# Performance work log

Hardware: AMD Instinct MI355X
Metric: run time of the kernel (lower is better)

## Reference

```python
import jax, jax.numpy as jnp
import numpy as np

B, T, C = 4, 4096, 512
H, KS = 8, 9
D = C // H
PAD = KS // 2


def setup_inputs() -> dict:
    key = jax.random.key(0)
    ks = jax.random.split(key, 9)
    s = 1.0 / np.sqrt(C)
    return {
        "x": jax.random.normal(ks[0], (B, T, C), jnp.float32),
        "Wq": jax.random.normal(ks[1], (C, C), jnp.float32) * s,
        "bq": jax.random.normal(ks[2], (C,), jnp.float32) * 0.01,
        "Wk": jax.random.normal(ks[3], (C, C), jnp.float32) * s,
        "bk": jax.random.normal(ks[4], (C,), jnp.float32) * 0.01,
        "Wv": jax.random.normal(ks[5], (C, C), jnp.float32) * s,
        "bv": jax.random.normal(ks[6], (C,), jnp.float32) * 0.01,
        "Wo": jax.random.normal(ks[7], (C, C), jnp.float32) * s,
        "bo": jax.random.normal(ks[8], (C,), jnp.float32) * 0.01,
    }


def reference(x, Wq, bq, Wk, bk, Wv, bv, Wo, bo):
    Bx, Tx, Cx = x.shape
    # projections (torch Linear: x @ W.T + b), split heads -> (B,H,T,D)
    q = (x @ Wq.T + bq).reshape(Bx, Tx, H, D).transpose(0, 2, 1, 3)
    k = (x @ Wk.T + bk).reshape(Bx, Tx, H, D).transpose(0, 2, 1, 3)
    v = (x @ Wv.T + bv).reshape(Bx, Tx, H, D).transpose(0, 2, 1, 3)
    # replicate-pad along time (matches F.pad mode='replicate')
    k_pad = jnp.pad(k, ((0, 0), (0, 0), (PAD, PAD), (0, 0)), mode='edge')
    v_pad = jnp.pad(v, ((0, 0), (0, 0), (PAD, PAD), (0, 0)), mode='edge')
    # window gather indices: (T, KS) into padded time axis
    idx = jnp.arange(Tx)[:, None] + jnp.arange(KS)[None, :]
    k_unf = k_pad[:, :, idx, :]  # (B,H,T,KS,D)
    v_unf = v_pad[:, :, idx, :]  # (B,H,T,KS,D)
    scale = 1.0 / np.sqrt(D)
    scores = jnp.einsum('bhtd,bhtkd->bhtk', q, k_unf) * scale  # (B,H,T,KS)
    attn = jax.nn.softmax(scores, axis=-1)
    y = jnp.einsum('bhtk,bhtkd->bhtd', attn, v_unf)  # (B,H,T,D)
    y = y.transpose(0, 2, 1, 3).reshape(Bx, Tx, Cx)
    return y @ Wo.T + bo
```

## Files before the change

kernel.cpp:

```cpp
#include <hip/hip_runtime.h>
#include <hip/hip_bf16.h>

#define B_    4
#define T_    4096
#define C_    512
#define H_    8
#define D_    64
#define KS_   9
#define PAD_  4
#define MTOT  (B_ * T_)
#define PLANE (MTOT * C_)
#define WU    (C_ * C_ / 8)

typedef __bf16 bf16_t;
typedef __bf16 bf16x8 __attribute__((ext_vector_type(8)));
typedef float  f32x4  __attribute__((ext_vector_type(4)));
typedef unsigned int  uint2v __attribute__((ext_vector_type(2)));

__global__ __launch_bounds__(256)
void conv_all(const float* __restrict__ Wq, const float* __restrict__ Wk,
              const float* __restrict__ Wv, const float* __restrict__ Wo,
              const float* __restrict__ x,
              bf16_t* __restrict__ Wb, bf16_t* __restrict__ xb) {
  int i = blockIdx.x * 256 + threadIdx.x;
  const float* src;
  bf16_t* dst;
  if (i < 4 * WU) {
    int w = i >> 15;
    const float* W = (w == 0) ? Wq : (w == 1) ? Wk : (w == 2) ? Wv : Wo;
    src = W + (size_t)(i & (WU - 1)) * 8;
    dst = Wb + (size_t)i * 8;
  } else {
    size_t j = (size_t)(i - 4 * WU);
    src = x + j * 8;
    dst = xb + j * 8;
  }
  float4 f0 = ((const float4*)src)[0];
  float4 f1 = ((const float4*)src)[1];
  bf16x8 o;
  o[0] = (bf16_t)f0.x; o[1] = (bf16_t)f0.y; o[2] = (bf16_t)f0.z; o[3] = (bf16_t)f0.w;
  o[4] = (bf16_t)f1.x; o[5] = (bf16_t)f1.y; o[6] = (bf16_t)f1.z; o[7] = (bf16_t)f1.w;
  *(bf16x8*)dst = o;
}

#define BM   128
#define BN   128
#define BK   32
#define NKT  (C_ / BK)
#define ASL  (BM * BK)
#define SLOT (2 * ASL)

#define GLD(srcp, off) __builtin_amdgcn_global_load_lds(                     \
    (const __attribute__((address_space(1))) unsigned int*)(srcp),           \
    (__attribute__((address_space(3))) unsigned int*)(&sm[off]), 16, 0, 0)

template<int MODE>
__global__ __launch_bounds__(256, 4)
void gemm8p(const bf16_t* __restrict__ A, const bf16_t* __restrict__ Bw,
            const float* __restrict__ b0, const float* __restrict__ b1,
            const float* __restrict__ b2, void* __restrict__ Outp) {
  __shared__ __align__(16) bf16_t sm[2 * SLOT];

  constexpr int GX  = (MODE == 0) ? (3 * C_ / BN) : (C_ / BN);
  constexpr int NWG = GX * (MTOT / BM);
  constexpr int CPX = NWG / 8;

  const int ord = blockIdx.y * GX + blockIdx.x;
  const int lg  = (ord & 7) * CPX + (ord >> 3);
  const int n0  = (lg % GX) * BN;
  const int m0  = (lg / GX) * BM;

  const int tid  = threadIdx.x;
  const int lane = tid & 63;
  const int wave = tid >> 6;
  const int wm   = wave >> 1;
  const int wn   = wave & 1;
  const int lr   = lane & 15;
  const int lq   = lane >> 4;

  const bf16_t* aSrc[2];
  const bf16_t* bSrc[2];
#pragma unroll
  for (int s = 0; s < 2; ++s) {
    int u = s * 256 + tid, r = u >> 2, sl = u & 3;
    int cs = (sl ^ ((r >> 1) & 3)) << 3;
    if constexpr (MODE == 0) {
      aSrc[s] = A + (size_t)(m0 + r) * C_ + cs;
    } else {
      int bb = m0 >> 12, t0 = m0 & (T_ - 1);
      aSrc[s] = A + ((size_t)bb * H_ * T_ + t0 + r) * D_ + cs;
    }
    bSrc[s] = Bw + (size_t)(n0 + r) * C_ + cs;
  }
  auto ofsA = [](int kt) -> size_t {
    if constexpr (MODE == 0) return (size_t)kt * BK;
    else return (size_t)(kt >> 1) * ((size_t)T_ * D_) + (size_t)(kt & 1) * 32;
  };

#pragma unroll
  for (int s = 0; s < 2; ++s) GLD(aSrc[s] + ofsA(0), (s * 256 + tid) * 8);
#pragma unroll
  for (int s = 0; s < 2; ++s) GLD(bSrc[s], ASL + (s * 256 + tid) * 8);
  asm volatile("s_waitcnt vmcnt(0)" ::: "memory");
  __builtin_amdgcn_s_barrier();

  f32x4 acc[4][4] = {};
  const int co = ((lq ^ ((lr >> 1) & 3)) << 3);

#pragma unroll
  for (int kt = 0; kt < NKT; ++kt) {
    const int rsl = kt & 1;
    const int wof = ((kt + 1) & 1) * SLOT;
    const bf16_t* abase = &sm[rsl * SLOT + (wm * 64 + lr) * BK + co];
    const bf16_t* bbase = &sm[rsl * SLOT + ASL + (wn * 64 + lr) * BK + co];

    bf16x8 af[4], bfr[4];
#pragma unroll
    for (int i = 0; i < 4; ++i) {
      af[i]  = *(const bf16x8*)(abase + i * (16 * BK));
      bfr[i] = *(const bf16x8*)(bbase + i * (16 * BK));
    }
    if (kt + 1 < NKT) {
#pragma unroll
      for (int s = 0; s < 2; ++s)
        GLD(aSrc[s] + ofsA(kt + 1), wof + (s * 256 + tid) * 8);
#pragma unroll
      for (int s = 0; s < 2; ++s)
        GLD(bSrc[s] + (size_t)(kt + 1) * BK, wof + ASL + (s * 256 + tid) * 8);
    }
    __builtin_amdgcn_s_setprio(1);
#pragma unroll
    for (int i = 0; i < 4; ++i)
#pragma unroll
      for (int j = 0; j < 4; ++j)
        acc[i][j] = __builtin_amdgcn_mfma_f32_16x16x32_bf16(
            bfr[j], af[i], acc[i][j], 0, 0, 0);
    __builtin_amdgcn_s_setprio(0);
    if (kt + 1 < NKT) {
      asm volatile("s_waitcnt vmcnt(0)" ::: "memory");
      __builtin_amdgcn_s_barrier();
    }
  }

  const int tl = lane & 15;
  const int dq = (lane >> 4) << 2;
  if constexpr (MODE == 0) {
    const int z  = n0 >> 9;
    const float* bias = (z == 0) ? b0 : (z == 1) ? b1 : b2;
    const int bb = m0 >> 12;
    const int t0 = m0 & (T_ - 1);
    bf16_t* plane = (bf16_t*)Outp + (size_t)z * PLANE;
#pragma unroll
    for (int j = 0; j < 4; ++j) {
      const int cc = (n0 & (C_ - 1)) + wn * 64 + j * 16 + dq;
      const int hh = cc >> 6, dd = cc & 63;
      const float4 bq4 = *(const float4*)(bias + cc);
      bf16_t* hb = plane + ((size_t)(bb * H_ + hh) * T_) * D_ + dd;
#pragma unroll
      for (int i = 0; i < 4; ++i) {
        const int t = t0 + wm * 64 + i * 16 + tl;
        bf16_t v0 = (bf16_t)(acc[i][j][0] + bq4.x);
        bf16_t v1 = (bf16_t)(acc[i][j][1] + bq4.y);
        bf16_t v2 = (bf16_t)(acc[i][j][2] + bq4.z);
        bf16_t v3 = (bf16_t)(acc[i][j][3] + bq4.w);
        unsigned int lo = ((unsigned short*)&v0)[0] |
                          ((unsigned int)((unsigned short*)&v1)[0] << 16);
        unsigned int hi = ((unsigned short*)&v2)[0] |
                          ((unsigned int)((unsigned short*)&v3)[0] << 16);
        uint2v pk; pk[0] = lo; pk[1] = hi;
        *(uint2v*)(hb + (size_t)t * D_) = pk;
      }
    }
  } else {
    float* outp = (float*)Outp;
#pragma unroll
    for (int j = 0; j < 4; ++j) {
      const int n = n0 + wn * 64 + j * 16 + dq;
      const float4 bq4 = *(const float4*)(b0 + n);
#pragma unroll
      for (int i = 0; i < 4; ++i) {
        const int m = m0 + wm * 64 + i * 16 + tl;
        float4 v;
        v.x = acc[i][j][0] + bq4.x;
        v.y = acc[i][j][1] + bq4.y;
        v.z = acc[i][j][2] + bq4.z;
        v.w = acc[i][j][3] + bq4.w;
        *(float4*)(outp + (size_t)m * C_ + n) = v;
      }
    }
  }
}

__global__ __launch_bounds__(256)
void attn_kernel(const bf16_t* __restrict__ qkv, bf16_t* __restrict__ y) {
  const int tid  = threadIdx.x;
  const int sub  = tid & 7;
  const int tl   = tid >> 3;
  const int t    = blockIdx.x * 32 + tl;
  const int h    = blockIdx.y;
  const int b    = blockIdx.z;

  const size_t pl = (size_t)(b * H_ + h) * T_ * D_;
  const bf16_t* q = qkv + pl;
  const bf16_t* k = qkv + (size_t)PLANE + pl;
  const bf16_t* v = qkv + (size_t)2 * PLANE + pl;
  const int c = sub * 8;

  int tj[KS_];
#pragma unroll
  for (int j = 0; j < KS_; ++j) {
    int tt = t - PAD_ + j;
    tj[j] = tt < 0 ? 0 : (tt >= T_ ? T_ - 1 : tt);
  }

  bf16x8 q8 = *(const bf16x8*)(q + (size_t)t * D_ + c);
  float qf[8];
#pragma unroll
  for (int e = 0; e < 8; ++e) qf[e] = (float)q8[e];

  float s[KS_];
#pragma unroll
  for (int j = 0; j < KS_; ++j) {
    bf16x8 k8 = *(const bf16x8*)(k + (size_t)tj[j] * D_ + c);
    float d0 = 0.f;
#pragma unroll
    for (int e = 0; e < 8; ++e) d0 += qf[e] * (float)k8[e];
    s[j] = d0;
  }

#pragma unroll
  for (int m = 1; m < 8; m <<= 1)
#pragma unroll
    for (int j = 0; j < KS_; ++j) s[j] += __shfl_xor(s[j], m, 8);

  float mx = s[0];
#pragma unroll
  for (int j = 1; j < KS_; ++j) mx = fmaxf(mx, s[j]);
  float w[KS_], sum = 0.f;
#pragma unroll
  for (int j = 0; j < KS_; ++j) {
    w[j] = __expf((s[j] - mx) * 0.125f);
    sum += w[j];
  }
  const float inv = 1.f / sum;
#pragma unroll
  for (int j = 0; j < KS_; ++j) w[j] *= inv;

  float o[8] = {0.f, 0.f, 0.f, 0.f, 0.f, 0.f, 0.f, 0.f};
#pragma unroll
  for (int j = 0; j < KS_; ++j) {
    bf16x8 v8 = *(const bf16x8*)(v + (size_t)tj[j] * D_ + c);
#pragma unroll
    for (int e = 0; e < 8; ++e) o[e] += w[j] * (float)v8[e];
  }
  bf16x8 o8;
#pragma unroll
  for (int e = 0; e < 8; ++e) o8[e] = (bf16_t)o[e];
  *(bf16x8*)(y + pl + (size_t)t * D_ + c) = o8;
}

extern "C" void kernel_launch(void* const* d_in, const int* in_sizes, int n_in,
                              void* d_out, int out_size, void* d_ws, size_t ws_size,
                              hipStream_t stream) {
  const float* x  = (const float*)d_in[0];
  const float* Wq = (const float*)d_in[1];
  const float* bq = (const float*)d_in[2];
  const float* Wk = (const float*)d_in[3];
  const float* bk = (const float*)d_in[4];
  const float* Wv = (const float*)d_in[5];
  const float* bv = (const float*)d_in[6];
  const float* Wo = (const float*)d_in[7];
  const float* bo = (const float*)d_in[8];
  float* out = (float*)d_out;

  bf16_t* Wb  = (bf16_t*)d_ws;
  bf16_t* xb  = Wb + (size_t)4 * C_ * C_;
  bf16_t* qkv = xb + (size_t)PLANE;
  bf16_t* y   = xb;

  conv_all<<<(4 * WU + PLANE / 8) / 256, 256, 0, stream>>>(Wq, Wk, Wv, Wo, x, Wb, xb);
  gemm8p<0><<<dim3(3 * C_ / BN, MTOT / BM), 256, 0, stream>>>(
      xb, Wb, bq, bk, bv, qkv);
  attn_kernel<<<dim3(T_ / 32, H_, B_), 256, 0, stream>>>(qkv, y);
  gemm8p<1><<<dim3(C_ / BN, MTOT / BM), 256, 0, stream>>>(
      y, Wb + (size_t)3 * C_ * C_, bo, nullptr, nullptr, out);
}
```

Measured before the change: 172.2 us.

## Give each wave private LDS tiles to drop block barriers in GEMM

Each wave now loads its own 64-row A and 64-row B slices into a private double-buffered LDS region, with two stages in flight, instead of sharing block-wide tiles. This removes the per-k-step s_barrier and the full vmcnt(0) drain, replacing them with a partial vmcnt wait. The cost is redundant global loads, since waves in the same row or column fetch the same data twice, and four times the LDS per block, so launch bounds drop occupancy from 4 to 2 blocks per CU.

```diff
diff --git a/kernel.cpp b/kernel.cpp
--- a/kernel.cpp
+++ b/kernel.cpp
@@ -47,19 +47,18 @@
 #define BN   128
 #define BK   32
 #define NKT  (C_ / BK)
-#define ASL  (BM * BK)
-#define SLOT (2 * ASL)
+#define WSL  4096
 
 #define GLD(srcp, off) __builtin_amdgcn_global_load_lds(                     \
     (const __attribute__((address_space(1))) unsigned int*)(srcp),           \
     (__attribute__((address_space(3))) unsigned int*)(&sm[off]), 16, 0, 0)
 
 template<int MODE>
-__global__ __launch_bounds__(256, 4)
+__global__ __launch_bounds__(256, 2)
 void gemm8p(const bf16_t* __restrict__ A, const bf16_t* __restrict__ Bw,
             const float* __restrict__ b0, const float* __restrict__ b1,
             const float* __restrict__ b2, void* __restrict__ Outp) {
-  __shared__ __align__(16) bf16_t sm[2 * SLOT];
+  __shared__ __align__(16) bf16_t sm[4 * 2 * WSL];
 
   constexpr int GX  = (MODE == 0) ? (3 * C_ / BN) : (C_ / BN);
   constexpr int NWG = GX * (MTOT / BM);
@@ -77,56 +76,57 @@
   const int wn   = wave & 1;
   const int lr   = lane & 15;
   const int lq   = lane >> 4;
-
-  const bf16_t* aSrc[2];
-  const bf16_t* bSrc[2];
-#pragma unroll
-  for (int s = 0; s < 2; ++s) {
-    int u = s * 256 + tid, r = u >> 2, sl = u & 3;
-    int cs = (sl ^ ((r >> 1) & 3)) << 3;
+  const int wbase = wave * (2 * WSL);
+
+  const bf16_t* aSrc[4];
+  const bf16_t* bSrc[4];
+#pragma unroll
+  for (int s = 0; s < 4; ++s) {
+    int u = s * 64 + lane;
+    int r = u >> 2, ch = u & 3;
+    int cs = (ch ^ ((r >> 1) & 3)) << 3;
     if constexpr (MODE == 0) {
-      aSrc[s] = A + (size_t)(m0 + r) * C_ + cs;
+      aSrc[s] = A + (size_t)(m0 + wm * 64 + r) * C_ + cs;
     } else {
       int bb = m0 >> 12, t0 = m0 & (T_ - 1);
-      aSrc[s] = A + ((size_t)bb * H_ * T_ + t0 + r) * D_ + cs;
-    }
-    bSrc[s] = Bw + (size_t)(n0 + r) * C_ + cs;
+      aSrc[s] = A + ((size_t)bb * H_ * T_ + t0 + wm * 64 + r) * D_ + cs;
+    }
+    bSrc[s] = Bw + (size_t)(n0 + wn * 64 + r) * C_ + cs;
   }
   auto ofsA = [](int kt) -> size_t {
     if constexpr (MODE == 0) return (size_t)kt * BK;
     else return (size_t)(kt >> 1) * ((size_t)T_ * D_) + (size_t)(kt & 1) * 32;
   };
 
-#pragma unroll
-  for (int s = 0; s < 2; ++s) GLD(aSrc[s] + ofsA(0), (s * 256 + tid) * 8);
-#pragma unroll
-  for (int s = 0; s < 2; ++s) GLD(bSrc[s], ASL + (s * 256 + tid) * 8);
-  asm volatile("s_waitcnt vmcnt(0)" ::: "memory");
-  __builtin_amdgcn_s_barrier();
+#define STAGE(kt, sl) do {                                                   \
+    _Pragma("unroll")                                                        \
+    for (int s_ = 0; s_ < 4; ++s_)                                           \
+      GLD(aSrc[s_] + ofsA(kt), wbase + (sl) * WSL + (s_ * 64 + lane) * 8);   \
+    _Pragma("unroll")                                                        \
+    for (int s_ = 0; s_ < 4; ++s_)                                           \
+      GLD(bSrc[s_] + (size_t)(kt) * BK,                                      \
+          wbase + (sl) * WSL + 2048 + (s_ * 64 + lane) * 8);                 \
+  } while (0)
+
+  STAGE(0, 0);
+  STAGE(1, 1);
 
   f32x4 acc[4][4] = {};
   const int co = ((lq ^ ((lr >> 1) & 3)) << 3);
 
 #pragma unroll
   for (int kt = 0; kt < NKT; ++kt) {
-    const int rsl = kt & 1;
-    const int wof = ((kt + 1) & 1) * SLOT;
-    const bf16_t* abase = &sm[rsl * SLOT + (wm * 64 + lr) * BK + co];
-    const bf16_t* bbase = &sm[rsl * SLOT + ASL + (wn * 64 + lr) * BK + co];
-
+    if (kt < NKT - 1) asm volatile("s_waitcnt vmcnt(8)" ::: "memory");
+    else              asm volatile("s_waitcnt vmcnt(0)" ::: "memory");
+    __builtin_amdgcn_sched_barrier(0);
+
+    const bf16_t* ab = &sm[wbase + (kt & 1) * WSL + lr * BK + co];
+    const bf16_t* bb2 = &sm[wbase + (kt & 1) * WSL + 2048 + lr * BK + co];
     bf16x8 af[4], bfr[4];
 #pragma unroll
     for (int i = 0; i < 4; ++i) {
-      af[i]  = *(const bf16x8*)(abase + i * (16 * BK));
-      bfr[i] = *(const bf16x8*)(bbase + i * (16 * BK));
-    }
-    if (kt + 1 < NKT) {
-#pragma unroll
-      for (int s = 0; s < 2; ++s)
-        GLD(aSrc[s] + ofsA(kt + 1), wof + (s * 256 + tid) * 8);
-#pragma unroll
-      for (int s = 0; s < 2; ++s)
-        GLD(bSrc[s] + (size_t)(kt + 1) * BK, wof + ASL + (s * 256 + tid) * 8);
+      af[i]  = *(const bf16x8*)(ab + i * (16 * BK));
+      bfr[i] = *(const bf16x8*)(bb2 + i * (16 * BK));
     }
     __builtin_amdgcn_s_setprio(1);
 #pragma unroll
@@ -136,11 +136,10 @@
         acc[i][j] = __builtin_amdgcn_mfma_f32_16x16x32_bf16(
             bfr[j], af[i], acc[i][j], 0, 0, 0);
     __builtin_amdgcn_s_setprio(0);
-    if (kt + 1 < NKT) {
-      asm volatile("s_waitcnt vmcnt(0)" ::: "memory");
-      __builtin_amdgcn_s_barrier();
-    }
-  }
+    __builtin_amdgcn_sched_barrier(0);
+    if (kt + 2 < NKT) STAGE(kt + 2, kt & 1);
+  }
+#undef STAGE
 
   const int tl = lane & 15;
   const int dq = (lane >> 4) << 2;
```

Measured after the change: 181.3 us. +5.3%, slower.
